# Performance work log

Hardware: AMD Instinct MI355X
Metric: run time of the kernel (lower is better)

## Reference

```python
import jax, jax.numpy as jnp
import numpy as np

K = 512
RATE = 0.999

def _l2norm(v):
    # matches torch F.normalize(dim=1): v / max(||v||, 1e-12)
    n = jnp.linalg.norm(v, axis=1, keepdims=True)
    return v / jnp.maximum(n, 1e-12)

def setup_inputs() -> dict:
    key = jax.random.key(0)
    k1, k2 = jax.random.split(key)
    x = jax.random.normal(k1, (16, 256, 64, 64), dtype=jnp.float32)
    m = jax.random.normal(k2, (K, 256), dtype=jnp.float32)
    return {"x": x, "m": m}

def reference(x, m):
    b, c, h, w = x.shape
    xf = x.transpose(0, 2, 3, 1).reshape(-1, c)          # (n, c)
    xn = _l2norm(xf)
    mn = _l2norm(m)
    score = xn @ mn.T                                     # (n, k)
    # EMA codebook update (uses detached x in the original)
    xd = jax.lax.stop_gradient(xf)
    embed_ind = jnp.argmax(score, axis=1)                 # (n,)
    embed_sum = jax.ops.segment_sum(xd, embed_ind, num_segments=K)   # (k, c)
    counts = jax.ops.segment_sum(jnp.ones(xd.shape[0], xd.dtype), embed_ind, num_segments=K)
    embed_mean = embed_sum / (counts[:, None] + 1e-6)
    new_m = m * RATE + embed_mean * (1.0 - RATE)          # (k, c)
    # re-score against updated codebook
    mn2 = _l2norm(new_m)
    score2 = xn @ mn2.T                                   # (n, k)
    soft_label = jax.nn.softmax(score2, axis=1)
    out = soft_label @ new_m                              # (n, c)
    out = out.reshape(b, h, w, c).transpose(0, 3, 1, 2)   # (b, c, h, w)
    return out, score2
```

## Files before the change

### kernel.cpp

```cpp
#include <hip/hip_runtime.h>

#define Bb 16
#define Cc 256
#define HW 4096
#define Nn 65536
#define Kk 512

typedef __attribute__((ext_vector_type(4))) float f32x4;
typedef __attribute__((ext_vector_type(8))) short short8;

__device__ __forceinline__ float bf2f(unsigned int u){
  union { float f; unsigned int i; } v; v.i = u << 16; return v.f;
}
__device__ __forceinline__ unsigned short f2bf(float f){
  unsigned int i = __float_as_uint(f);
  unsigned int r = (i + 0x7fffu + ((i >> 16) & 1u)) >> 16;
  return (unsigned short)r;
}


__global__ __launch_bounds__(64) void k_mnorm(const float* __restrict__ m,
                                              unsigned short* __restrict__ mnf){
  int k = blockIdx.x, l = threadIdx.x;
  float4 v = *reinterpret_cast<const float4*>(m + (size_t)k * Cc + l * 4);
  float ss = v.x*v.x + v.y*v.y + v.z*v.z + v.w*v.w;
  #pragma unroll
  for (int off = 1; off < 64; off <<= 1) ss += __shfl_xor(ss, off, 64);
  float rn = 1.0f / fmaxf(sqrtf(ss), 1e-12f);
  ushort4 o;
  o.x = f2bf(v.x*rn); o.y = f2bf(v.y*rn); o.z = f2bf(v.z*rn); o.w = f2bf(v.w*rn);
  int kw = k >> 6, kt = (k >> 4) & 3, li = k & 15;
  int c0 = l * 4;
  int ks = c0 >> 5, gr = (c0 >> 3) & 3, eo = (l & 1) * 4;
  size_t off8 = ((((size_t)(kw*4 + kt)*8 + ks)*16 + li)*4 + gr)*8 + eo;
  *reinterpret_cast<ushort4*>(mnf + off8) = o;
}

__global__ __launch_bounds__(512, 4) void k_prep_score(const float* __restrict__ x,
                                                       const unsigned short* __restrict__ mnf,
                                                       float* __restrict__ rs,
                                                       unsigned short* __restrict__ xr,
                                                       int* __restrict__ eind){
  __shared__ __align__(16) char ldsB[32768];
  __shared__ float red[8][64];
  __shared__ float smax[8][64];
  __shared__ int   sidx[8][64];
  int t = threadIdx.x, w = t >> 6, l = t & 63, gr = l >> 4, li = l & 15;
  int b = blockIdx.x >> 6;
  int hw0 = (blockIdx.x & 63) << 6;
  const float* src = x + ((size_t)b * Cc + w * 32) * HW + hw0 + l;
  float ss = 0.f;
  unsigned int pk[16];
  #pragma unroll
  for (int j = 0; j < 16; ++j){
    float v0 = src[(size_t)(2*j    ) * HW];
    float v1 = src[(size_t)(2*j + 1) * HW];
    ss += v0 * v0 + v1 * v1;
    pk[j] = (unsigned int)f2bf(v0) | ((unsigned int)f2bf(v1) << 16);
  }
  #pragma unroll
  for (int q = 0; q < 4; ++q){
    int colb = w * 64 + q * 16;
    int4 vv;
    vv.x = (int)pk[q*4+0]; vv.y = (int)pk[q*4+1];
    vv.z = (int)pk[q*4+2]; vv.w = (int)pk[q*4+3];
    *reinterpret_cast<int4*>(ldsB + l * 512 + (colb ^ ((l & 7) << 4))) = vv;
  }
  red[w][l] = ss;
  __syncthreads();
  if (t < 64){
    float s = 0.f;
    #pragma unroll
    for (int ww = 0; ww < 8; ++ww) s += red[ww][t];
    rs[(size_t)b * HW + hw0 + t] = 1.0f / fmaxf(sqrtf(s), 1e-12f);
  }
  f32x4 acc[4][4];
  #pragma unroll
  for (int mt = 0; mt < 4; ++mt)
    #pragma unroll
    for (int nt = 0; nt < 4; ++nt)
      acc[mt][nt] = (f32x4){0.f,0.f,0.f,0.f};
  int loff = li * 32 + gr * 8;
  for (int ks = 0; ks < 8; ++ks){
    short8 af[4];
    #pragma unroll
    for (int mt = 0; mt < 4; ++mt){
      int row = mt * 16 + li;
      af[mt] = *reinterpret_cast<const short8*>(
          ldsB + row * 512 + ((ks * 64 + gr * 16) ^ ((row & 7) << 4)));
    }
    #pragma unroll
    for (int nt = 0; nt < 4; ++nt){
      short8 bv = *reinterpret_cast<const short8*>(
          mnf + ((size_t)(w*4 + nt)*8 + ks)*512 + loff);
      #pragma unroll
      for (int mt = 0; mt < 4; ++mt)
        acc[mt][nt] = __builtin_amdgcn_mfma_f32_16x16x32_bf16(af[mt], bv, acc[mt][nt], 0, 0, 0);
    }
  }
  #pragma unroll
  for (int mt = 0; mt < 4; ++mt){
    #pragma unroll
    for (int r = 0; r < 4; ++r){
      float best = acc[mt][0][r]; int bi = w * 64 + li;
      #pragma unroll
      for (int nt = 1; nt < 4; ++nt){
        float v = acc[mt][nt][r]; int ii = w * 64 + nt * 16 + li;
        if (v > best){ best = v; bi = ii; }
      }
      #pragma unroll
      for (int off = 1; off < 16; off <<= 1){
        float ov = __shfl_xor(best, off, 64);
        int   oi = __shfl_xor(bi,   off, 64);
        if (ov > best || (ov == best && oi < bi)){ best = ov; bi = oi; }
      }
      if (li == 0){ int pr = mt * 16 + gr * 4 + r; smax[w][pr] = best; sidx[w][pr] = bi; }
    }
  }
  __syncthreads();
  if (t < 64){
    float best = smax[0][t]; int bi = sidx[0][t];
    #pragma unroll
    for (int ww = 1; ww < 8; ++ww){
      float v = smax[ww][t]; int ii = sidx[ww][t];
      if (v > best || (v == best && ii < bi)){ best = v; bi = ii; }
    }
    eind[(size_t)b * HW + hw0 + t] = bi;
  }
  char* dst = reinterpret_cast<char*>(xr) + ((size_t)b * HW + hw0) * 512;
  #pragma unroll
  for (int i = 0; i < 4; ++i){
    int px = i * 16 + (t >> 5);
    int colb = (t & 31) * 16;
    int4 rv = *reinterpret_cast<const int4*>(ldsB + px * 512 + (colb ^ ((px & 7) << 4)));
    *reinterpret_cast<int4*>(dst + (size_t)px * 512 + colb) = rv;
  }
}

__global__ __launch_bounds__(256) void k_segsum(const int* __restrict__ eind,
                                                const unsigned short* __restrict__ xr,
                                                float* __restrict__ es4,
                                                float* __restrict__ ec4){
  int kk = blockIdx.x >> 2, qr = blockIdx.x & 3;
  int t = threadIdx.x, w = t >> 6, l = t & 63;
  float a0=0.f,a1=0.f,a2=0.f,a3=0.f;
  int cnt = 0;
  int base = qr * 16384 + w * 4096;
  for (int it = 0; it < 16; ++it){
    int pxb = base + it * 256;
    int4 e = *reinterpret_cast<const int4*>(eind + pxb + l * 4);
    #pragma unroll
    for (int comp = 0; comp < 4; ++comp){
      int ev = comp == 0 ? e.x : comp == 1 ? e.y : comp == 2 ? e.z : e.w;
      unsigned long long mask = __ballot(ev == kk);
      cnt += (int)__popcll(mask);
      while (mask){
        int src = __ffsll((unsigned long long)mask) - 1;
        mask &= mask - 1;
        int px = pxb + src * 4 + comp;
        ushort4 uv = *reinterpret_cast<const ushort4*>(xr + (size_t)px * Cc + l * 4);
        a0 += bf2f(uv.x); a1 += bf2f(uv.y);
        a2 += bf2f(uv.z); a3 += bf2f(uv.w);
      }
    }
  }
  __shared__ float red[4][256];
  __shared__ float rcnt[4];
  red[w][l*4+0]=a0; red[w][l*4+1]=a1; red[w][l*4+2]=a2; red[w][l*4+3]=a3;
  if (l == 0) rcnt[w] = (float)cnt;
  __syncthreads();
  float s = red[0][t] + red[1][t] + red[2][t] + red[3][t];
  es4[(size_t)blockIdx.x * Cc + t] = s;
  if (t == 0) ec4[blockIdx.x] = rcnt[0] + rcnt[1] + rcnt[2] + rcnt[3];
}

__global__ __launch_bounds__(64) void k_update(const float* __restrict__ es4,
                                               const float* __restrict__ ec4,
                                               const float* __restrict__ m,
                                               unsigned short* __restrict__ mn2f,
                                               unsigned short* __restrict__ nmTf){
  int k = blockIdx.x, l = threadIdx.x;
  float sx = 0.f, sy = 0.f, sz = 0.f, sw = 0.f, cs = 0.f;
  #pragma unroll
  for (int q = 0; q < 4; ++q){
    float4 s = *reinterpret_cast<const float4*>(es4 + ((size_t)(4*k+q)) * Cc + l * 4);
    sx += s.x; sy += s.y; sz += s.z; sw += s.w;
    cs += ec4[4*k+q];
  }
  float4 mv = *reinterpret_cast<const float4*>(m + (size_t)k * Cc + l * 4);
  float inv = 1.0f / (cs + 1e-6f);
  float nx = mv.x * 0.999f + sx * inv * 0.001f;
  float ny = mv.y * 0.999f + sy * inv * 0.001f;
  float nz = mv.z * 0.999f + sz * inv * 0.001f;
  float nw = mv.w * 0.999f + sw * inv * 0.001f;
  float ss = nx*nx + ny*ny + nz*nz + nw*nw;
  #pragma unroll
  for (int off = 1; off < 64; off <<= 1) ss += __shfl_xor(ss, off, 64);
  float rn = 1.0f / fmaxf(sqrtf(ss), 1e-12f);
  ushort4 o;
  o.x = f2bf(nx*rn); o.y = f2bf(ny*rn); o.z = f2bf(nz*rn); o.w = f2bf(nw*rn);
  {
    int kw = k >> 6, kt = (k >> 4) & 3, li = k & 15;
    int c0 = l * 4;
    int ks = c0 >> 5, gr = (c0 >> 3) & 3, eo = (l & 1) * 4;
    size_t off8 = ((((size_t)(kw*4 + kt)*8 + ks)*16 + li)*4 + gr)*8 + eo;
    *reinterpret_cast<ushort4*>(mn2f + off8) = o;
  }
  {
    int ksn = k >> 5, grn = (k >> 3) & 3, en = k & 7;
    unsigned short nv[4] = {f2bf(nx), f2bf(ny), f2bf(nz), f2bf(nw)};
    #pragma unroll
    for (int q = 0; q < 4; ++q){
      int c = l * 4 + q;
      int cb = c >> 4, li2 = c & 15;
      size_t off8 = ((((size_t)cb*16 + ksn)*16 + li2)*4 + grn)*8 + en;
      nmTf[off8] = nv[q];
    }
  }
}

__global__ __launch_bounds__(512, 2) void k_out(const unsigned short* __restrict__ xr,
                                                const float* __restrict__ rs,
                                                const unsigned short* __restrict__ mn2f,
                                                const unsigned short* __restrict__ nmTf,
                                                float* __restrict__ out,
                                                float* __restrict__ score2){
  __shared__ __align__(16) char smem[131072];
  __shared__ float wbuf[8 * 128];
  __shared__ float rz[128];
  __shared__ float rsl[128];
  int t = threadIdx.x, w = t >> 6, l = t & 63, gr = l >> 4, li = l & 15;
  int px0 = blockIdx.x * 128;
  const char* gsrc = reinterpret_cast<const char*>(xr + (size_t)px0 * Cc);
  #pragma unroll
  for (int j = 0; j < 8; ++j){
    int chunk = j * 512 + t;
    int rr = chunk >> 5, slot = chunk & 31;
    int4 v = *reinterpret_cast<const int4*>(gsrc + rr * 512 + slot * 16);
    *reinterpret_cast<int4*>(smem + rr * 512 + ((slot * 16) ^ ((rr & 7) << 4))) = v;
  }
  if (t < 128) rsl[t] = rs[px0 + t];
  __syncthreads();
  f32x4 acc[4][8];
  #pragma unroll
  for (int kt = 0; kt < 4; ++kt)
    #pragma unroll
    for (int pt = 0; pt < 8; ++pt)
      acc[kt][pt] = (f32x4){0.f,0.f,0.f,0.f};
  int kw = w * 64;
  int loff = li * 32 + gr * 8;
  for (int ks = 0; ks < 8; ++ks){
    short8 am[4];
    #pragma unroll
    for (int kt = 0; kt < 4; ++kt)
      am[kt] = *reinterpret_cast<const short8*>(
          mn2f + ((size_t)(w*4 + kt)*8 + ks)*512 + loff);
    #pragma unroll
    for (int pt = 0; pt < 8; ++pt){
      int row = pt * 16 + li;
      short8 bx = *reinterpret_cast<const short8*>(
          smem + row * 512 + ((ks * 64 + gr * 16) ^ ((row & 7) << 4)));
      #pragma unroll
      for (int kt = 0; kt < 4; ++kt)
        acc[kt][pt] = __builtin_amdgcn_mfma_f32_16x16x32_bf16(am[kt], bx, acc[kt][pt], 0, 0, 0);
    }
  }
  __syncthreads();
  float s[8] = {0.f,0.f,0.f,0.f,0.f,0.f,0.f,0.f};
  #pragma unroll
  for (int kt = 0; kt < 4; ++kt){
    #pragma unroll
    for (int pt = 0; pt < 8; ++pt){
      int px = pt * 16 + li;
      float rsv = rsl[px];
      f32x4 v = acc[kt][pt];
      v[0] *= rsv; v[1] *= rsv; v[2] *= rsv; v[3] *= rsv;
      acc[kt][pt] = v;
      float p0 = __expf(v[0]), p1 = __expf(v[1]), p2 = __expf(v[2]), p3 = __expf(v[3]);
      s[pt] += (p0 + p1) + (p2 + p3);
      unsigned int lo = (unsigned int)f2bf(p0) | ((unsigned int)f2bf(p1) << 16);
      unsigned int hi = (unsigned int)f2bf(p2) | ((unsigned int)f2bf(p3) << 16);
      int colb = (kw + kt * 16 + gr * 4) * 2;
      uint2 pv; pv.x = lo; pv.y = hi;
      *reinterpret_cast<uint2*>(smem + px * 1024 + (colb ^ ((px & 7) << 4))) = pv;
    }
  }
  #pragma unroll
  for (int pt = 0; pt < 8; ++pt){
    s[pt] += __shfl_xor(s[pt], 16, 64);
    s[pt] += __shfl_xor(s[pt], 32, 64);
  }
  if (gr == 0){
    #pragma unroll
    for (int pt = 0; pt < 8; ++pt) wbuf[w * 128 + pt * 16 + li] = s[pt];
  }
  __syncthreads();
  if (t < 128){
    float sum = 0.f;
    #pragma unroll
    for (int ww = 0; ww < 8; ++ww) sum += wbuf[ww * 128 + t];
    rz[t] = 1.0f / sum;
  }
  f32x4 acc2[8][2];
  #pragma unroll
  for (int mt = 0; mt < 8; ++mt)
    #pragma unroll
    for (int nt = 0; nt < 2; ++nt)
      acc2[mt][nt] = (f32x4){0.f,0.f,0.f,0.f};
  for (int ks = 0; ks < 16; ++ks){
    short8 bv[2];
    #pragma unroll
    for (int nt = 0; nt < 2; ++nt)
      bv[nt] = *reinterpret_cast<const short8*>(
          nmTf + ((size_t)(w*2 + nt)*16 + ks)*512 + loff);
    #pragma unroll
    for (int mt = 0; mt < 8; ++mt){
      int row = mt * 16 + li;
      short8 af = *reinterpret_cast<const short8*>(
          smem + row * 1024 + ((ks * 64 + gr * 16) ^ ((row & 7) << 4)));
      #pragma unroll
      for (int nt = 0; nt < 2; ++nt)
        acc2[mt][nt] = __builtin_amdgcn_mfma_f32_16x16x32_bf16(af, bv[nt], acc2[mt][nt], 0, 0, 0);
    }
  }
  __syncthreads();
  float* s2 = score2 + (size_t)px0 * Kk;
  #pragma unroll
  for (int h = 0; h < 2; ++h){
    #pragma unroll
    for (int kt = 0; kt < 4; ++kt)
      #pragma unroll
      for (int pt2 = 0; pt2 < 4; ++pt2){
        int pxl = pt2 * 16 + li;
        int kb = (kw + kt * 16 + gr * 4) * 4;
        *reinterpret_cast<f32x4*>(smem + pxl * 2048 + (kb ^ ((pxl & 7) << 4)))
            = acc[kt][h * 4 + pt2];
      }
    __syncthreads();
    #pragma unroll
    for (int r = 0; r < 8; ++r){
      int pxl = w * 8 + r;
      int px = h * 64 + pxl;
      #pragma unroll
      for (int j = 0; j < 2; ++j){
        int o = j * 1024 + l * 16;
        f32x4 v = *reinterpret_cast<const f32x4*>(smem + pxl * 2048 + (o ^ ((pxl & 7) << 4)));
        *reinterpret_cast<f32x4*>(s2 + (size_t)px * Kk + (o >> 2)) = v;
      }
    }
    __syncthreads();
  }
  #pragma unroll
  for (int mt = 0; mt < 8; ++mt){
    int pb = mt * 16 + gr * 4;
    f32x4 rzv = *reinterpret_cast<const f32x4*>(&rz[pb]);
    #pragma unroll
    for (int nt = 0; nt < 2; ++nt){
      int c = w * 32 + nt * 16 + li;
      f32x4 v;
      v[0] = acc2[mt][nt][0] * rzv[0];
      v[1] = acc2[mt][nt][1] * rzv[1];
      v[2] = acc2[mt][nt][2] * rzv[2];
      v[3] = acc2[mt][nt][3] * rzv[3];
      *reinterpret_cast<f32x4*>(smem + c * 512 + ((pb * 4) ^ ((c & 7) << 4))) = v;
    }
  }
  __syncthreads();
  int b = px0 >> 12, hw0 = px0 & 4095;
  #pragma unroll
  for (int i = 0; i < 16; ++i){
    int c = w * 32 + i * 2 + (l >> 5);
    int o = (l & 31) * 16;
    f32x4 v = *reinterpret_cast<const f32x4*>(smem + c * 512 + (o ^ ((c & 7) << 4)));
    *reinterpret_cast<f32x4*>(out + ((size_t)b * Cc + c) * HW + hw0 + (o >> 2)) = v;
  }
}

extern "C" void kernel_launch(void* const* d_in, const int* in_sizes, int n_in,
                              void* d_out, int out_size, void* d_ws, size_t ws_size,
                              hipStream_t stream) {
  (void)in_sizes; (void)n_in; (void)out_size; (void)ws_size;
  const float* x = (const float*)d_in[0];
  const float* m = (const float*)d_in[1];
  float* out    = (float*)d_out;
  float* score2 = (float*)d_out + (size_t)Nn * Cc;

  char* ws = (char*)d_ws;
  unsigned short* xr   = (unsigned short*)(ws);
  float*          rsb  = (float*)(ws + 33554432);
  unsigned short* mnf  = (unsigned short*)(ws + 33816576);
  int*            ei   = (int*)(ws + 34078720);
  float*          es4  = (float*)(ws + 34340864);
  float*          ec4  = (float*)(ws + 36438016);
  unsigned short* mn2f = (unsigned short*)(ws + 36446208);
  unsigned short* nmTf = (unsigned short*)(ws + 36708352);

  k_mnorm       <<<512,  64,  0, stream>>>(m, mnf);
  k_prep_score  <<<1024, 512, 0, stream>>>(x, mnf, rsb, xr, ei);
  k_segsum      <<<2048, 256, 0, stream>>>(ei, xr, es4, ec4);
  k_update      <<<512,  64,  0, stream>>>(es4, ec4, m, mn2f, nmTf);
  k_out         <<<512,  512, 0, stream>>>(xr, rsb, mn2f, nmTf, out, score2);
}
```

Before: 153.6 us.

## Prefetch codebook fragments one k-step ahead and stage x tile via direct global-to-LDS loads

The codebook operand fragments in the score, output and argmax kernels are now loaded one k-step ahead into registers (double-buffered) and the first fragment is issued before the barrier, so global latency overlaps MFMA work. The x tile load in k_out now uses the global_load_lds builtin with the swizzle applied on the source address, skipping the trip through registers. Loops are fully unrolled. The cost is higher register pressure under launch_bounds(512,2), with a risk of spills or lower occupancy.

```diff
diff --git a/kernel.cpp b/kernel.cpp
--- a/kernel.cpp
+++ b/kernel.cpp
@@ -16,6 +16,17 @@
   unsigned int i = __float_as_uint(f);
   unsigned int r = (i + 0x7fffu + ((i >> 16) & 1u)) >> 16;
   return (unsigned short)r;
+}
+
+__device__ __forceinline__ void gld_lds16(const char* g, char* lbase){
+#if __has_builtin(__builtin_amdgcn_global_load_lds)
+  __builtin_amdgcn_global_load_lds(
+      (const __attribute__((address_space(1))) unsigned int*)g,
+      (__attribute__((address_space(3))) unsigned int*)lbase, 16, 0, 0);
+#else
+  *reinterpret_cast<int4*>(lbase + (threadIdx.x & 63) * 16) =
+      *reinterpret_cast<const int4*>(g);
+#endif
 }
 
 
@@ -67,6 +78,12 @@
     *reinterpret_cast<int4*>(ldsB + l * 512 + (colb ^ ((l & 7) << 4))) = vv;
   }
   red[w][l] = ss;
+  int loff = li * 32 + gr * 8;
+  short8 bv0[4];
+  #pragma unroll
+  for (int nt = 0; nt < 4; ++nt)
+    bv0[nt] = *reinterpret_cast<const short8*>(
+        mnf + ((size_t)(w*4 + nt)*8 + 0)*512 + loff);
   __syncthreads();
   if (t < 64){
     float s = 0.f;
@@ -80,7 +97,7 @@
     #pragma unroll
     for (int nt = 0; nt < 4; ++nt)
       acc[mt][nt] = (f32x4){0.f,0.f,0.f,0.f};
-  int loff = li * 32 + gr * 8;
+  #pragma unroll
   for (int ks = 0; ks < 8; ++ks){
     short8 af[4];
     #pragma unroll
@@ -91,8 +108,9 @@
     }
     #pragma unroll
     for (int nt = 0; nt < 4; ++nt){
-      short8 bv = *reinterpret_cast<const short8*>(
-          mnf + ((size_t)(w*4 + nt)*8 + ks)*512 + loff);
+      short8 bv = (ks == 0) ? bv0[nt]
+          : *reinterpret_cast<const short8*>(
+                mnf + ((size_t)(w*4 + nt)*8 + ks)*512 + loff);
       #pragma unroll
       for (int mt = 0; mt < 4; ++mt)
         acc[mt][nt] = __builtin_amdgcn_mfma_f32_16x16x32_bf16(af[mt], bv, acc[mt][nt], 0, 0, 0);
@@ -236,9 +254,16 @@
   for (int j = 0; j < 8; ++j){
     int chunk = j * 512 + t;
     int rr = chunk >> 5, slot = chunk & 31;
-    int4 v = *reinterpret_cast<const int4*>(gsrc + rr * 512 + slot * 16);
-    *reinterpret_cast<int4*>(smem + rr * 512 + ((slot * 16) ^ ((rr & 7) << 4))) = v;
-  }
+    const char* g = gsrc + rr * 512 + ((slot * 16) ^ ((rr & 7) << 4));
+    int rr0 = (j * 512 + w * 64) >> 5;
+    gld_lds16(g, smem + rr0 * 512);
+  }
+  int loff = li * 32 + gr * 8;
+  short8 amc[4];
+  #pragma unroll
+  for (int kt = 0; kt < 4; ++kt)
+    amc[kt] = *reinterpret_cast<const short8*>(
+        mn2f + ((size_t)(w*4 + kt)*8 + 0)*512 + loff);
   if (t < 128) rsl[t] = rs[px0 + t];
   __syncthreads();
   f32x4 acc[4][8];
@@ -248,13 +273,15 @@
     for (int pt = 0; pt < 8; ++pt)
       acc[kt][pt] = (f32x4){0.f,0.f,0.f,0.f};
   int kw = w * 64;
-  int loff = li * 32 + gr * 8;
+  #pragma unroll
   for (int ks = 0; ks < 8; ++ks){
-    short8 am[4];
-    #pragma unroll
-    for (int kt = 0; kt < 4; ++kt)
-      am[kt] = *reinterpret_cast<const short8*>(
-          mn2f + ((size_t)(w*4 + kt)*8 + ks)*512 + loff);
+    short8 amn[4];
+    if (ks < 7){
+      #pragma unroll
+      for (int kt = 0; kt < 4; ++kt)
+        amn[kt] = *reinterpret_cast<const short8*>(
+            mn2f + ((size_t)(w*4 + kt)*8 + (ks+1))*512 + loff);
+    }
     #pragma unroll
     for (int pt = 0; pt < 8; ++pt){
       int row = pt * 16 + li;
@@ -262,7 +289,11 @@
           smem + row * 512 + ((ks * 64 + gr * 16) ^ ((row & 7) << 4)));
       #pragma unroll
       for (int kt = 0; kt < 4; ++kt)
-        acc[kt][pt] = __builtin_amdgcn_mfma_f32_16x16x32_bf16(am[kt], bx, acc[kt][pt], 0, 0, 0);
+        acc[kt][pt] = __builtin_amdgcn_mfma_f32_16x16x32_bf16(amc[kt], bx, acc[kt][pt], 0, 0, 0);
+    }
+    if (ks < 7){
+      #pragma unroll
+      for (int kt = 0; kt < 4; ++kt) amc[kt] = amn[kt];
     }
   }
   __syncthreads();
@@ -294,6 +325,11 @@
     #pragma unroll
     for (int pt = 0; pt < 8; ++pt) wbuf[w * 128 + pt * 16 + li] = s[pt];
   }
+  short8 bvc[2];
+  #pragma unroll
+  for (int nt = 0; nt < 2; ++nt)
+    bvc[nt] = *reinterpret_cast<const short8*>(
+        nmTf + ((size_t)(w*2 + nt)*16 + 0)*512 + loff);
   __syncthreads();
   if (t < 128){
     float sum = 0.f;
@@ -307,12 +343,15 @@
     #pragma unroll
     for (int nt = 0; nt < 2; ++nt)
       acc2[mt][nt] = (f32x4){0.f,0.f,0.f,0.f};
+  #pragma unroll
   for (int ks = 0; ks < 16; ++ks){
-    short8 bv[2];
-    #pragma unroll
-    for (int nt = 0; nt < 2; ++nt)
-      bv[nt] = *reinterpret_cast<const short8*>(
-          nmTf + ((size_t)(w*2 + nt)*16 + ks)*512 + loff);
+    short8 bvn[2];
+    if (ks < 15){
+      #pragma unroll
+      for (int nt = 0; nt < 2; ++nt)
+        bvn[nt] = *reinterpret_cast<const short8*>(
+            nmTf + ((size_t)(w*2 + nt)*16 + (ks+1))*512 + loff);
+    }
     #pragma unroll
     for (int mt = 0; mt < 8; ++mt){
       int row = mt * 16 + li;
@@ -320,7 +359,11 @@
           smem + row * 1024 + ((ks * 64 + gr * 16) ^ ((row & 7) << 4)));
       #pragma unroll
       for (int nt = 0; nt < 2; ++nt)
-        acc2[mt][nt] = __builtin_amdgcn_mfma_f32_16x16x32_bf16(af, bv[nt], acc2[mt][nt], 0, 0, 0);
+        acc2[mt][nt] = __builtin_amdgcn_mfma_f32_16x16x32_bf16(af, bvc[nt], acc2[mt][nt], 0, 0, 0);
+    }
+    if (ks < 15){
+      #pragma unroll
+      for (int nt = 0; nt < 2; ++nt) bvc[nt] = bvn[nt];
     }
   }
   __syncthreads();
```

Measured after the change: 149.7 us, median of 2. -2.5%, faster.
